# Optimization experiments

Hardware: AMD Instinct MI355X
Metric: run time of the kernel (lower is better)

Reference implementation:

```python
import jax, jax.numpy as jnp
import numpy as np

N_LEVELS = 16
N_FEATS = 2
LOG2_T = 19
TABLE_SIZE = 1 << LOG2_T
BASE_RES = 16
FINEST_RES = 512
DIM = 3
N_POINTS = 2_000_000
PRIMES = jnp.array([1, 2654435761, 805459861], dtype=jnp.uint32)


def _hash_encode(x01, tables, resolutions):
    """Multi-resolution hash grid encoding with trilinear interpolation.
    x01: [N, D] in [0, 1]; tables: [L, T, F]; resolutions: [L] float.
    Returns [N, L*F]."""
    N, D = x01.shape
    T = tables.shape[1]
    # all 2^D corner offsets of the enclosing voxel, shape [2^D, D]
    offsets = jnp.array([[(i >> d) & 1 for d in range(D)] for i in range(1 << D)],
                        dtype=jnp.float32)

    def per_level(table, res):
        pos = x01 * res                      # [N, D]
        p0 = jnp.floor(pos)
        w = pos - p0                         # fractional part, [N, D]
        corners = p0[None, :, :] + offsets[:, None, :]      # [2^D, N, D]
        ci = corners.astype(jnp.uint32)
        hp = ci * PRIMES[None, None, :D]                    # uint32 wraps mod 2^32
        h = hp[..., 0]
        for d in range(1, D):
            h = h ^ hp[..., d]
        idx = (h & jnp.uint32(T - 1)).astype(jnp.int32)     # [2^D, N]
        feats = table[idx]                                  # gather, [2^D, N, F]
        # trilinear weights: prod_d (w_d if corner bit set else 1-w_d)
        wc = jnp.prod(jnp.where(offsets[:, None, :] > 0, w[None], 1.0 - w[None]),
                      axis=-1)                              # [2^D, N]
        return jnp.sum(wc[..., None] * feats, axis=0)       # [N, F]

    f = jax.vmap(per_level)(tables, resolutions)            # [L, N, F]
    return jnp.transpose(f, (1, 0, 2)).reshape(N, -1)       # [N, L*F]


def setup_inputs() -> dict:
    key = jax.random.key(0)
    ks = jax.random.split(key, 8)
    x = jax.random.uniform(ks[0], (N_POINTS, DIM), jnp.float32, -1.0, 1.0)
    tables = jax.random.uniform(ks[1], (N_LEVELS, TABLE_SIZE, N_FEATS),
                                jnp.float32, -1e-4, 1e-4)
    b = np.exp((np.log(FINEST_RES) - np.log(BASE_RES)) / (N_LEVELS - 1))
    resolutions = jnp.asarray(np.floor(BASE_RES * b ** np.arange(N_LEVELS)),
                              dtype=jnp.float32)
    in_dim = N_LEVELS * N_FEATS  # 32
    W1 = jax.random.normal(ks[2], (in_dim, 64), jnp.float32) * (1.0 / np.sqrt(in_dim))
    b1 = jnp.zeros((64,), jnp.float32)
    W2 = jax.random.normal(ks[3], (64, 64), jnp.float32) * (1.0 / 8.0)
    b2 = jnp.zeros((64,), jnp.float32)
    W3 = jax.random.normal(ks[4], (64, 1), jnp.float32) * (1.0 / 8.0)
    b3 = jnp.zeros((1,), jnp.float32)
    return {"x": x, "tables": tables, "resolutions": resolutions,
            "W1": W1, "b1": b1, "W2": W2, "b2": b2, "W3": W3, "b3": b3}


def reference(x, tables, resolutions, W1, b1, W2, b2, W3, b3):
    x01 = x / 2.0 + 0.5                       # map [-1,1] -> [0,1]
    a = _hash_encode(x01, tables, resolutions)  # [N, 32]
    h = jax.nn.relu(a @ W1 + b1)
    h = jax.nn.relu(h @ W2 + b2)
    return h @ W3 + b3                        # [N, 1]
```

## Files before the change

kernel.cpp:

```cpp
#include <hip/hip_runtime.h>
#include <hip/hip_bf16.h>
#include <stdint.h>

#define N_LEVELS   16
#define LOG2_T     19
#define TABLE_SIZE (1u << LOG2_T)
#define PRIME_Y    2654435761u
#define PRIME_Z    805459861u

#define NB        32768
#define SORT_B    256

typedef float v4f __attribute__((ext_vector_type(4)));
typedef _Float16 v8h __attribute__((ext_vector_type(8)));

__device__ __forceinline__ uint32_t part1by2(uint32_t v) {
    v &= 0x3FFu;
    v = (v | (v << 16)) & 0x030000FFu;
    v = (v | (v <<  8)) & 0x0300F00Fu;
    v = (v | (v <<  4)) & 0x030C30C3u;
    v = (v | (v <<  2)) & 0x09249249u;
    return v;
}
__device__ __forceinline__ uint32_t morton_key(float xr, float yr, float zr) {
    int vx = (int)((xr * 0.5f + 0.5f) * 32.0f);
    int vy = (int)((yr * 0.5f + 0.5f) * 32.0f);
    int vz = (int)((zr * 0.5f + 0.5f) * 32.0f);
    vx = vx < 0 ? 0 : (vx > 31 ? 31 : vx);
    vy = vy < 0 ? 0 : (vy > 31 ? 31 : vy);
    vz = vz < 0 ? 0 : (vz > 31 ? 31 : vz);
    return part1by2((uint32_t)vx) | (part1by2((uint32_t)vy) << 1)
         | (part1by2((uint32_t)vz) << 2);
}

__global__ __launch_bounds__(256)
void hist_kernel(const float* __restrict__ x, uint32_t* __restrict__ g_hist,
                 int n, int chunk)
{
    __shared__ uint32_t pack[NB / 2];
    const int b = blockIdx.x, t = threadIdx.x;
    for (int w = t; w < NB / 2; w += 256) pack[w] = 0;
    __syncthreads();
    const int beg = b * chunk;
    const int end = (beg + chunk < n) ? (beg + chunk) : n;
    for (int i = beg + t; i < end; i += 256) {
        const uint32_t key = morton_key(x[3*i], x[3*i+1], x[3*i+2]);
        atomicAdd(&pack[key >> 1], 1u << ((key & 1u) << 4));
    }
    __syncthreads();
    uint32_t* __restrict__ dst = g_hist + (size_t)b * NB;
    for (int w = t; w < NB / 2; w += 256) {
        const uint32_t p = pack[w];
        dst[2*w]     = p & 0xFFFFu;
        dst[2*w + 1] = p >> 16;
    }
}

__global__ __launch_bounds__(256)
void scan_cols_kernel(const uint32_t* __restrict__ g_hist,
                      uint32_t* __restrict__ g_part,
                      uint32_t* __restrict__ totals)
{
    const int key = blockIdx.x * 256 + threadIdx.x;
    uint32_t run = 0;
    #pragma unroll 8
    for (int b = 0; b < SORT_B; ++b) {
        const size_t idx = (size_t)b * NB + key;
        const uint32_t v = g_hist[idx];
        g_part[idx] = run;
        run += v;
    }
    totals[key] = run;
}

__global__ void scan_block_kernel(const uint32_t* __restrict__ counts,
                                  uint32_t* __restrict__ prefix,
                                  uint32_t* __restrict__ blocksum) {
    __shared__ uint32_t s[256];
    const int t = threadIdx.x;
    const int i = blockIdx.x * 256 + t;
    const uint32_t v = counts[i];
    s[t] = v; __syncthreads();
    #pragma unroll
    for (int d = 1; d < 256; d <<= 1) {
        const uint32_t u = (t >= d) ? s[t - d] : 0;
        __syncthreads();
        s[t] += u;
        __syncthreads();
    }
    prefix[i] = s[t] - v;
    if (t == 255) blocksum[blockIdx.x] = s[255];
}

__global__ void scan_top_kernel(const uint32_t* __restrict__ blocksum,
                                uint32_t* __restrict__ blockbase, int nb) {
    __shared__ uint32_t s[1024];
    const int t = threadIdx.x;
    const uint32_t v = (t < nb) ? blocksum[t] : 0;
    s[t] = v; __syncthreads();
    #pragma unroll
    for (int d = 1; d < 1024; d <<= 1) {
        const uint32_t u = (t >= d) ? s[t - d] : 0;
        __syncthreads();
        s[t] += u;
        __syncthreads();
    }
    if (t < nb) blockbase[t] = s[t] - v;
}

__global__ void addback_kernel(const uint32_t* __restrict__ prefix,
                               const uint32_t* __restrict__ blockbase,
                               uint32_t* __restrict__ base) {
    const int i = blockIdx.x * 256 + threadIdx.x;
    base[i] = prefix[i] + blockbase[i >> 8];
}

__global__ __launch_bounds__(256)
void scatter_kernel(const float* __restrict__ x,
                    const uint32_t* __restrict__ base,
                    const uint32_t* __restrict__ g_part,
                    float* __restrict__ xs,
                    int* __restrict__ rank_inv,
                    int n, int chunk)
{
    __shared__ uint32_t pack[NB / 2];
    const int b = blockIdx.x, t = threadIdx.x;
    for (int w = t; w < NB / 2; w += 256) pack[w] = 0;
    __syncthreads();
    const uint32_t* __restrict__ part = g_part + (size_t)b * NB;
    const int beg = b * chunk;
    const int end = (beg + chunk < n) ? (beg + chunk) : n;
    for (int i = beg + t; i < end; i += 256) {
        const float a = x[3*i], c = x[3*i+1], d = x[3*i+2];
        const uint32_t key = morton_key(a, c, d);
        const uint32_t sh = (key & 1u) << 4;
        uint32_t r = atomicAdd(&pack[key >> 1], 1u << sh);
        r = (r >> sh) & 0xFFFFu;
        const uint32_t pos = base[key] + part[key] + r;
        xs[pos]         = a;
        xs[n + pos]     = c;
        xs[2*n + pos]   = d;
        rank_inv[i]     = (int)pos;
    }
}

__global__ __launch_bounds__(256, 8)
void encode_kernel(const float* __restrict__ xs,
                   const float* __restrict__ tables,
                   const float* __restrict__ resolutions,
                   _Float16* __restrict__ a_ws,
                   int n)
{
    const int l = blockIdx.y;
    int p = blockIdx.x * blockDim.x + threadIdx.x;
    if (p >= n) p = n - 1;

    const float x0 = xs[p]       * 0.5f + 0.5f;
    const float x1 = xs[n + p]   * 0.5f + 0.5f;
    const float x2 = xs[2*n + p] * 0.5f + 0.5f;

    const float res = resolutions[l];
    const float px = x0 * res, py = x1 * res, pz = x2 * res;
    const float fx = floorf(px), fy = floorf(py), fz = floorf(pz);
    const float wx = px - fx, wy = py - fy, wz = pz - fz;
    const uint32_t cx = (uint32_t)fx;
    const uint32_t cy = (uint32_t)fy;
    const uint32_t cz = (uint32_t)fz;

    const uint32_t hy0 = cy * PRIME_Y, hy1 = hy0 + PRIME_Y;
    const uint32_t hz0 = cz * PRIME_Z, hz1 = hz0 + PRIME_Z;

    const float wx0 = 1.0f - wx, wy0 = 1.0f - wy, wz0 = 1.0f - wz;

    const float* __restrict__ tab = tables + (size_t)l * (size_t)TABLE_SIZE * 2u;

    const uint32_t hyz[4] = { hy0 ^ hz0, hy1 ^ hz0, hy0 ^ hz1, hy1 ^ hz1 };

    float2 cva[4], cvb[4];

    if ((cx & 1u) == 0u) {
        #pragma unroll
        for (int q = 0; q < 4; ++q) {
            const uint32_t idx_a = (cx ^ hyz[q]) & (TABLE_SIZE - 1u);
            const uint32_t base  = idx_a & ~1u;
            const float4 f4 = *(const float4*)(tab + 2u * base);
            const bool hi = (idx_a & 1u) != 0u;
            cva[q] = hi ? make_float2(f4.z, f4.w) : make_float2(f4.x, f4.y);
            cvb[q] = hi ? make_float2(f4.x, f4.y) : make_float2(f4.z, f4.w);
        }
    } else {
        const uint32_t hx0 = cx, hx1 = cx + 1u;
        #pragma unroll
        for (int q = 0; q < 4; ++q) {
            const uint32_t idx_a = (hx0 ^ hyz[q]) & (TABLE_SIZE - 1u);
            const uint32_t idx_b = (hx1 ^ hyz[q]) & (TABLE_SIZE - 1u);
            cva[q] = *(const float2*)(tab + 2u * idx_a);
            cvb[q] = *(const float2*)(tab + 2u * idx_b);
        }
    }

    float f0 = 0.0f, f1 = 0.0f;
    #pragma unroll
    for (int q = 0; q < 4; ++q) {
        const float yf = (q & 1) ? wy : wy0;
        const float zf = (q & 2) ? wz : wz0;
        const float wgt_a = (wx0 * yf) * zf;
        const float wgt_b = (wx  * yf) * zf;
        f0 = fmaf(wgt_a, cva[q].x, f0);
        f1 = fmaf(wgt_a, cva[q].y, f1);
        f0 = fmaf(wgt_b, cvb[q].x, f0);
        f1 = fmaf(wgt_b, cvb[q].y, f1);
    }

    a_ws[(size_t)(2 * l + 0) * n + p] = (_Float16)(f0 * 256.0f);
    a_ws[(size_t)(2 * l + 1) * n + p] = (_Float16)(f1 * 256.0f);
}

__global__ __launch_bounds__(256, 2)
void mlp_mfma_kernel(const _Float16* __restrict__ a_ws,
                     const float* __restrict__ W1,
                     const float* __restrict__ b1,
                     const float* __restrict__ W2,
                     const float* __restrict__ b2,
                     const float* __restrict__ W3,
                     const float* __restrict__ b3,
                     float* __restrict__ outs,
                     int n)
{
    __shared__ float lds[4 * 64 * 16];

    const int lane    = threadIdx.x & 63;
    const int wave_id = threadIdx.x >> 6;
    const int m       = lane & 15;
    const int q       = lane >> 4;
    float* __restrict__ myl = &lds[wave_id * 1024];

    const float b3s = b3[0];

    v8h a1[4];
    #pragma unroll
    for (int t = 0; t < 4; ++t)
        #pragma unroll
        for (int j = 0; j < 8; ++j)
            a1[t][j] = (_Float16)W1[(8 * q + j) * 64 + 16 * t + m];

    v8h a2[2][4];
    #pragma unroll
    for (int c = 0; c < 2; ++c)
        #pragma unroll
        for (int t = 0; t < 4; ++t)
            #pragma unroll
            for (int j = 0; j < 8; ++j)
                a2[c][t][j] = (_Float16)W2[(32 * c + 8 * q + j) * 64 + 16 * t + m];

    float bias1v[16], bias2v[16], w3v[16];
    #pragma unroll
    for (int t = 0; t < 4; ++t)
        #pragma unroll
        for (int r = 0; r < 4; ++r) {
            const int ch = 16 * t + 4 * q + r;
            bias1v[4 * t + r] = 256.0f * b1[ch];
            bias2v[4 * t + r] = 256.0f * b2[ch];
            w3v[4 * t + r]    = W3[ch];
        }

    const int nt = (n + 15) >> 4;
    const int stride = gridDim.x * 4;
    const int gw = blockIdx.x * 4 + wave_id;
    if (gw >= nt) return;

    v8h bh;
    {
        const int p0 = gw * 16;
        const int pr = (p0 + m < n) ? (p0 + m) : (n - 1);
        #pragma unroll
        for (int j = 0; j < 8; ++j)
            bh[j] = a_ws[(size_t)(8 * q + j) * n + pr];
    }

    for (int tile = gw; tile < nt; tile += stride) {
        const int p0 = tile * 16;

        v8h bhn = bh;
        const int nx = tile + stride;
        if (nx < nt) {
            const int p0n = nx * 16;
            const int prn = (p0n + m < n) ? (p0n + m) : (n - 1);
            #pragma unroll
            for (int j = 0; j < 8; ++j)
                bhn[j] = a_ws[(size_t)(8 * q + j) * n + prn];
        }

        v4f acc1[4];
        #pragma unroll
        for (int t = 0; t < 4; ++t) {
            #pragma unroll
            for (int r = 0; r < 4; ++r) acc1[t][r] = bias1v[4 * t + r];
            acc1[t] = __builtin_amdgcn_mfma_f32_16x16x32_f16(a1[t], bh, acc1[t], 0, 0, 0);
        }

        #pragma unroll
        for (int t = 0; t < 4; ++t)
            #pragma unroll
            for (int r = 0; r < 4; ++r)
                myl[(16 * t + 4 * q + r) * 16 + m] = fmaxf(acc1[t][r], 0.0f);
        __threadfence_block();

        v8h b2h[2];
        #pragma unroll
        for (int c = 0; c < 2; ++c)
            #pragma unroll
            for (int j = 0; j < 8; ++j)
                b2h[c][j] = (_Float16)myl[(32 * c + 8 * q + j) * 16 + m];

        v4f acc2[4];
        #pragma unroll
        for (int t = 0; t < 4; ++t) {
            #pragma unroll
            for (int r = 0; r < 4; ++r) acc2[t][r] = bias2v[4 * t + r];
            acc2[t] = __builtin_amdgcn_mfma_f32_16x16x32_f16(a2[0][t], b2h[0], acc2[t], 0, 0, 0);
            acc2[t] = __builtin_amdgcn_mfma_f32_16x16x32_f16(a2[1][t], b2h[1], acc2[t], 0, 0, 0);
        }

        float partial = 0.0f;
        #pragma unroll
        for (int t = 0; t < 4; ++t)
            #pragma unroll
            for (int r = 0; r < 4; ++r)
                partial = fmaf(fmaxf(acc2[t][r], 0.0f), w3v[4 * t + r], partial);

        partial += __shfl_xor(partial, 16);
        partial += __shfl_xor(partial, 32);

        if (q == 0 && p0 + m < n)
            outs[p0 + m] = partial * (1.0f / 256.0f) + b3s;

        bh = bhn;
    }
}

__global__ void unscatter_kernel(const float* __restrict__ outs,
                                 const int* __restrict__ rank_inv,
                                 float* __restrict__ out, int n) {
    const int i = blockIdx.x * blockDim.x + threadIdx.x;
    if (i < n) out[i] = outs[rank_inv[i]];
}

__global__ __launch_bounds__(256, 4)
void hashgrid_mlp_fused(const float* __restrict__ x,
                        const float* __restrict__ tables,
                        const float* __restrict__ resolutions,
                        const float* __restrict__ W1,
                        const float* __restrict__ b1,
                        const float* __restrict__ W2,
                        const float* __restrict__ b2,
                        const float* __restrict__ W3,
                        const float* __restrict__ b3,
                        float* __restrict__ out,
                        int n)
{
    const int i  = blockIdx.x * blockDim.x + threadIdx.x;
    const int ip = (i < n) ? i : (n - 1);

    const float x0 = x[3 * ip + 0] * 0.5f + 0.5f;
    const float x1 = x[3 * ip + 1] * 0.5f + 0.5f;
    const float x2 = x[3 * ip + 2] * 0.5f + 0.5f;

    float h1[64];
    #pragma unroll
    for (int j = 0; j < 64; ++j) h1[j] = b1[j];

    #pragma unroll
    for (int l = 0; l < N_LEVELS; ++l) {
        const float res = resolutions[l];
        const float px = x0 * res, py = x1 * res, pz = x2 * res;
        const float fx = floorf(px), fy = floorf(py), fz = floorf(pz);
        const float wx = px - fx, wy = py - fy, wz = pz - fz;
        const uint32_t cx = (uint32_t)fx;
        const uint32_t cy = (uint32_t)fy;
        const uint32_t cz = (uint32_t)fz;
        const uint32_t hx0 = cx,           hx1 = cx + 1u;
        const uint32_t hy0 = cy * PRIME_Y, hy1 = hy0 + PRIME_Y;
        const uint32_t hz0 = cz * PRIME_Z, hz1 = hz0 + PRIME_Z;
        const float wx0 = 1.0f - wx, wy0 = 1.0f - wy, wz0 = 1.0f - wz;
        const float* __restrict__ tab = tables + (size_t)l * (size_t)TABLE_SIZE * 2u;

        float f0 = 0.0f, f1 = 0.0f;
        #pragma unroll
        for (int c = 0; c < 8; ++c) {
            const uint32_t h = ((c & 1) ? hx1 : hx0) ^
                               ((c & 2) ? hy1 : hy0) ^
                               ((c & 4) ? hz1 : hz0);
            const uint32_t idx = h & (TABLE_SIZE - 1u);
            const float2 fv = *(const float2*)(tab + 2u * idx);
            const float wgt = ((c & 1) ? wx : wx0) *
                              ((c & 2) ? wy : wy0) *
                              ((c & 4) ? wz : wz0);
            f0 = fmaf(wgt, fv.x, f0);
            f1 = fmaf(wgt, fv.y, f1);
        }
        const float* __restrict__ w1a = W1 + (2 * l + 0) * 64;
        const float* __restrict__ w1b = W1 + (2 * l + 1) * 64;
        #pragma unroll
        for (int j = 0; j < 64; ++j)
            h1[j] = fmaf(f1, w1b[j], fmaf(f0, w1a[j], h1[j]));
    }

    #pragma unroll
    for (int j = 0; j < 64; ++j) h1[j] = fmaxf(h1[j], 0.0f);

    float accum = b3[0];
    #pragma unroll
    for (int half = 0; half < 2; ++half) {
        float h2[32];
        #pragma unroll
        for (int j = 0; j < 32; ++j) h2[j] = b2[half * 32 + j];
        #pragma unroll
        for (int k = 0; k < 64; ++k) {
            const float hk = h1[k];
            const float* __restrict__ w2row = W2 + k * 64 + half * 32;
            #pragma unroll
            for (int j = 0; j < 32; ++j)
                h2[j] = fmaf(hk, w2row[j], h2[j]);
        }
        #pragma unroll
        for (int j = 0; j < 32; ++j)
            accum = fmaf(fmaxf(h2[j], 0.0f), W3[half * 32 + j], accum);
    }
    out[ip] = accum;
}

extern "C" void kernel_launch(void* const* d_in, const int* in_sizes, int n_in,
                              void* d_out, int out_size, void* d_ws, size_t ws_size,
                              hipStream_t stream) {
    const float* x           = (const float*)d_in[0];
    const float* tables      = (const float*)d_in[1];
    const float* resolutions = (const float*)d_in[2];
    const float* W1          = (const float*)d_in[3];
    const float* b1          = (const float*)d_in[4];
    const float* W2          = (const float*)d_in[5];
    const float* b2          = (const float*)d_in[6];
    const float* W3          = (const float*)d_in[7];
    const float* b3          = (const float*)d_in[8];
    float* out               = (float*)d_out;

    const int n = out_size;
    const int block = 256;
    const int grid_pts = (n + block - 1) / block;
    const int chunk = (n + SORT_B - 1) / SORT_B;

    size_t off = 0;
    #define CARVE(bytes) (off = (off + 255) & ~(size_t)255, off += (bytes), off - (bytes))
    const size_t aws_off   = CARVE((size_t)32 * n * sizeof(_Float16));
    const size_t xs_off    = CARVE((size_t)3 * n * sizeof(float));
    const size_t rank_off  = CARVE((size_t)n * sizeof(int));
    const size_t outs_off  = CARVE((size_t)n * sizeof(float));
    const size_t tot_off   = CARVE((size_t)NB * sizeof(uint32_t));
    const size_t pref_off  = CARVE((size_t)NB * sizeof(uint32_t));
    const size_t base_off  = CARVE((size_t)NB * sizeof(uint32_t));
    const size_t bsum_off  = CARVE(1024 * sizeof(uint32_t));
    const size_t bbase_off = CARVE(1024 * sizeof(uint32_t));
    const size_t total_ws  = off;
    #undef CARVE

    if (ws_size >= total_ws) {
        char* ws = (char*)d_ws;
        _Float16* a_ws   = (_Float16*)(ws + aws_off);
        uint32_t* g_hist = (uint32_t*)(ws + aws_off);
        uint32_t* g_part = (uint32_t*)(ws + aws_off + (size_t)SORT_B * NB * 4);
        float*    xs     = (float*)(ws + xs_off);
        int*      rank   = (int*)(ws + rank_off);
        float*    outs   = (float*)(ws + outs_off);
        uint32_t* totals = (uint32_t*)(ws + tot_off);
        uint32_t* pref   = (uint32_t*)(ws + pref_off);
        uint32_t* base   = (uint32_t*)(ws + base_off);
        uint32_t* bsum   = (uint32_t*)(ws + bsum_off);
        uint32_t* bbase  = (uint32_t*)(ws + bbase_off);

        hist_kernel<<<SORT_B, block, 0, stream>>>(x, g_hist, n, chunk);
        scan_cols_kernel<<<NB / 256, block, 0, stream>>>(g_hist, g_part, totals);
        scan_block_kernel<<<NB / 256, block, 0, stream>>>(totals, pref, bsum);
        scan_top_kernel<<<1, 1024, 0, stream>>>(bsum, bbase, NB / 256);
        addback_kernel<<<NB / 256, block, 0, stream>>>(pref, bbase, base);
        scatter_kernel<<<SORT_B, block, 0, stream>>>(x, base, g_part, xs, rank, n, chunk);

        dim3 grid_enc(grid_pts, N_LEVELS);
        encode_kernel<<<grid_enc, block, 0, stream>>>(xs, tables, resolutions, a_ws, n);
        mlp_mfma_kernel<<<1024, block, 0, stream>>>(a_ws, W1, b1, W2, b2, W3, b3, outs, n);
        unscatter_kernel<<<grid_pts, block, 0, stream>>>(outs, rank, out, n);
    } else {
        hashgrid_mlp_fused<<<grid_pts, block, 0, stream>>>(
            x, tables, resolutions, W1, b1, W2, b2, W3, b3, out, n);
    }
}
```

Measured before the change: 672.3 us.

## Merge prefix-scan kernels, fuse unscatter into MLP store, widen sort blocks

Replaces the three-kernel global prefix scan with one single-block scan in which each of 1024 threads handles 32 buckets. The scatter now records the original index per sorted position, so the MLP kernel writes straight to the final output location and the separate unscatter kernel is dropped. The histogram and scatter kernels go from 256 to 1024 threads per block. This removes three kernel launches and one full-size pass over the output and rank arrays, in exchange for scattered output writes from the MLP and more LDS atomic contention per block.

```diff
diff --git a/kernel.cpp b/kernel.cpp
--- a/kernel.cpp
+++ b/kernel.cpp
@@ -33,23 +33,23 @@
          | (part1by2((uint32_t)vz) << 2);
 }
 
-__global__ __launch_bounds__(256)
+__global__ __launch_bounds__(1024)
 void hist_kernel(const float* __restrict__ x, uint32_t* __restrict__ g_hist,
                  int n, int chunk)
 {
     __shared__ uint32_t pack[NB / 2];
     const int b = blockIdx.x, t = threadIdx.x;
-    for (int w = t; w < NB / 2; w += 256) pack[w] = 0;
+    for (int w = t; w < NB / 2; w += 1024) pack[w] = 0;
     __syncthreads();
     const int beg = b * chunk;
     const int end = (beg + chunk < n) ? (beg + chunk) : n;
-    for (int i = beg + t; i < end; i += 256) {
+    for (int i = beg + t; i < end; i += 1024) {
         const uint32_t key = morton_key(x[3*i], x[3*i+1], x[3*i+2]);
         atomicAdd(&pack[key >> 1], 1u << ((key & 1u) << 4));
     }
     __syncthreads();
     uint32_t* __restrict__ dst = g_hist + (size_t)b * NB;
-    for (int w = t; w < NB / 2; w += 256) {
+    for (int w = t; w < NB / 2; w += 1024) {
         const uint32_t p = pack[w];
         dst[2*w]     = p & 0xFFFFu;
         dst[2*w + 1] = p >> 16;
@@ -73,74 +73,57 @@
     totals[key] = run;
 }
 
-__global__ void scan_block_kernel(const uint32_t* __restrict__ counts,
-                                  uint32_t* __restrict__ prefix,
-                                  uint32_t* __restrict__ blocksum) {
-    __shared__ uint32_t s[256];
-    const int t = threadIdx.x;
-    const int i = blockIdx.x * 256 + t;
-    const uint32_t v = counts[i];
-    s[t] = v; __syncthreads();
-    #pragma unroll
-    for (int d = 1; d < 256; d <<= 1) {
-        const uint32_t u = (t >= d) ? s[t - d] : 0;
-        __syncthreads();
-        s[t] += u;
-        __syncthreads();
-    }
-    prefix[i] = s[t] - v;
-    if (t == 255) blocksum[blockIdx.x] = s[255];
-}
-
-__global__ void scan_top_kernel(const uint32_t* __restrict__ blocksum,
-                                uint32_t* __restrict__ blockbase, int nb) {
+__global__ __launch_bounds__(1024)
+void scan_full_kernel(const uint32_t* __restrict__ totals,
+                      uint32_t* __restrict__ base)
+{
     __shared__ uint32_t s[1024];
     const int t = threadIdx.x;
-    const uint32_t v = (t < nb) ? blocksum[t] : 0;
-    s[t] = v; __syncthreads();
-    #pragma unroll
+    const int beg = t * (NB / 1024);
+    uint32_t loc[NB / 1024];
+    #pragma unroll
+    for (int k = 0; k < NB / 1024; ++k) loc[k] = totals[beg + k];
+    uint32_t sum = 0;
+    #pragma unroll
+    for (int k = 0; k < NB / 1024; ++k) { const uint32_t v = loc[k]; loc[k] = sum; sum += v; }
+    s[t] = sum; __syncthreads();
     for (int d = 1; d < 1024; d <<= 1) {
         const uint32_t u = (t >= d) ? s[t - d] : 0;
         __syncthreads();
         s[t] += u;
         __syncthreads();
     }
-    if (t < nb) blockbase[t] = s[t] - v;
-}
-
-__global__ void addback_kernel(const uint32_t* __restrict__ prefix,
-                               const uint32_t* __restrict__ blockbase,
-                               uint32_t* __restrict__ base) {
-    const int i = blockIdx.x * 256 + threadIdx.x;
-    base[i] = prefix[i] + blockbase[i >> 8];
-}
-
-__global__ __launch_bounds__(256)
+    const uint32_t excl = s[t] - sum;
+    #pragma unroll
+    for (int k = 0; k < NB / 1024; ++k) base[beg + k] = loc[k] + excl;
+}
+
+__global__ __launch_bounds__(1024)
 void scatter_kernel(const float* __restrict__ x,
                     const uint32_t* __restrict__ base,
                     const uint32_t* __restrict__ g_part,
                     float* __restrict__ xs,
-                    int* __restrict__ rank_inv,
+                    int* __restrict__ pid,
                     int n, int chunk)
 {
     __shared__ uint32_t pack[NB / 2];
     const int b = blockIdx.x, t = threadIdx.x;
-    for (int w = t; w < NB / 2; w += 256) pack[w] = 0;
+    for (int w = t; w < NB / 2; w += 1024) pack[w] = 0;
     __syncthreads();
     const uint32_t* __restrict__ part = g_part + (size_t)b * NB;
     const int beg = b * chunk;
     const int end = (beg + chunk < n) ? (beg + chunk) : n;
-    for (int i = beg + t; i < end; i += 256) {
+    for (int i = beg + t; i < end; i += 1024) {
         const float a = x[3*i], c = x[3*i+1], d = x[3*i+2];
         const uint32_t key = morton_key(a, c, d);
         const uint32_t sh = (key & 1u) << 4;
         uint32_t r = atomicAdd(&pack[key >> 1], 1u << sh);
         r = (r >> sh) & 0xFFFFu;
         const uint32_t pos = base[key] + part[key] + r;
-        xs[pos]         = a;
-        xs[n + pos]     = c;
-        xs[2*n + pos]   = d;
-        rank_inv[i]     = (int)pos;
+        xs[pos]       = a;
+        xs[n + pos]   = c;
+        xs[2*n + pos] = d;
+        pid[pos]      = i;
     }
 }
 
@@ -218,13 +201,14 @@
 
 __global__ __launch_bounds__(256, 2)
 void mlp_mfma_kernel(const _Float16* __restrict__ a_ws,
+                     const int* __restrict__ pid,
                      const float* __restrict__ W1,
                      const float* __restrict__ b1,
                      const float* __restrict__ W2,
                      const float* __restrict__ b2,
                      const float* __restrict__ W3,
                      const float* __restrict__ b3,
-                     float* __restrict__ outs,
+                     float* __restrict__ out,
                      int n)
 {
     __shared__ float lds[4 * 64 * 16];
@@ -333,17 +317,10 @@
         partial += __shfl_xor(partial, 32);
 
         if (q == 0 && p0 + m < n)
-            outs[p0 + m] = partial * (1.0f / 256.0f) + b3s;
+            out[pid[p0 + m]] = partial * (1.0f / 256.0f) + b3s;
 
         bh = bhn;
     }
-}
-
-__global__ void unscatter_kernel(const float* __restrict__ outs,
-                                 const int* __restrict__ rank_inv,
-                                 float* __restrict__ out, int n) {
-    const int i = blockIdx.x * blockDim.x + threadIdx.x;
-    if (i < n) out[i] = outs[rank_inv[i]];
 }
 
 __global__ __launch_bounds__(256, 4)
@@ -453,13 +430,9 @@
     #define CARVE(bytes) (off = (off + 255) & ~(size_t)255, off += (bytes), off - (bytes))
     const size_t aws_off   = CARVE((size_t)32 * n * sizeof(_Float16));
     const size_t xs_off    = CARVE((size_t)3 * n * sizeof(float));
-    const size_t rank_off  = CARVE((size_t)n * sizeof(int));
-    const size_t outs_off  = CARVE((size_t)n * sizeof(float));
+    const size_t pid_off   = CARVE((size_t)n * sizeof(int));
     const size_t tot_off   = CARVE((size_t)NB * sizeof(uint32_t));
-    const size_t pref_off  = CARVE((size_t)NB * sizeof(uint32_t));
     const size_t base_off  = CARVE((size_t)NB * sizeof(uint32_t));
-    const size_t bsum_off  = CARVE(1024 * sizeof(uint32_t));
-    const size_t bbase_off = CARVE(1024 * sizeof(uint32_t));
     const size_t total_ws  = off;
     #undef CARVE
 
@@ -469,25 +442,18 @@
         uint32_t* g_hist = (uint32_t*)(ws + aws_off);
         uint32_t* g_part = (uint32_t*)(ws + aws_off + (size_t)SORT_B * NB * 4);
         float*    xs     = (float*)(ws + xs_off);
-        int*      rank   = (int*)(ws + rank_off);
-        float*    outs   = (float*)(ws + outs_off);
+        int*      pid    = (int*)(ws + pid_off);
         uint32_t* totals = (uint32_t*)(ws + tot_off);
-        uint32_t* pref   = (uint32_t*)(ws + pref_off);
         uint32_t* base   = (uint32_t*)(ws + base_off);
-        uint32_t* bsum   = (uint32_t*)(ws + bsum_off);
-        uint32_t* bbase  = (uint32_t*)(ws + bbase_off);
-
-        hist_kernel<<<SORT_B, block, 0, stream>>>(x, g_hist, n, chunk);
-        scan_cols_kernel<<<NB / 256, block, 0, stream>>>(g_hist, g_part, totals);
-        scan_block_kernel<<<NB / 256, block, 0, stream>>>(totals, pref, bsum);
-        scan_top_kernel<<<1, 1024, 0, stream>>>(bsum, bbase, NB / 256);
-        addback_kernel<<<NB / 256, block, 0, stream>>>(pref, bbase, base);
-        scatter_kernel<<<SORT_B, block, 0, stream>>>(x, base, g_part, xs, rank, n, chunk);
+
+        hist_kernel<<<SORT_B, 1024, 0, stream>>>(x, g_hist, n, chunk);
+        scan_cols_kernel<<<NB / 256, 256, 0, stream>>>(g_hist, g_part, totals);
+        scan_full_kernel<<<1, 1024, 0, stream>>>(totals, base);
+        scatter_kernel<<<SORT_B, 1024, 0, stream>>>(x, base, g_part, xs, pid, n, chunk);
 
         dim3 grid_enc(grid_pts, N_LEVELS);
         encode_kernel<<<grid_enc, block, 0, stream>>>(xs, tables, resolutions, a_ws, n);
-        mlp_mfma_kernel<<<1024, block, 0, stream>>>(a_ws, W1, b1, W2, b2, W3, b3, outs, n);
-        unscatter_kernel<<<grid_pts, block, 0, stream>>>(outs, rank, out, n);
+        mlp_mfma_kernel<<<1024, block, 0, stream>>>(a_ws, pid, W1, b1, W2, b2, W3, b3, out, n);
     } else {
         hashgrid_mlp_fused<<<grid_pts, block, 0, stream>>>(
             x, tables, resolutions, W1, b1, W2, b2, W3, b3, out, n);
```

Result: no change. 682.0 us (+1.4%).
